# Optimization experiments

Hardware: AMD Instinct MI355X
Metric: run time of the kernel (lower is better)

Reference implementation:

```python
import jax, jax.numpy as jnp
import numpy as np

# dims
B, N, T, F, D = 16, 64, 168, 8, 248   # batch, stations, seq, features, gcn_dim
E = D + F                              # transformer dmodel = 256
H = 8                                  # attention heads
FF = 4 * E                             # expansion_factor * dmodel


def _layer_norm(x, g, b, eps=1e-5):
    m = jnp.mean(x, axis=-1, keepdims=True)
    v = jnp.var(x, axis=-1, keepdims=True)
    return (x - m) * jax.lax.rsqrt(v + eps) * g + b


def setup_inputs() -> dict:
    key = jax.random.key(0)
    ks = jax.random.split(key, 20)
    s = 0.02
    return {
        'x': jax.random.normal(ks[0], (B, N, T, F), jnp.float32),
        'locs': jax.random.uniform(ks[1], (B, N, 2), jnp.float32),
        'pos_em': jax.random.normal(ks[2], (B, T, E), jnp.float32),
        'periodic_em': jax.random.normal(ks[3], (B, T, E), jnp.float32),
        'gcn_w': jax.random.normal(ks[4], (F, D), jnp.float32) * s,
        'gcn_b': jnp.zeros((D,), jnp.float32),
        'fc1_w': jax.random.normal(ks[5], (D, D), jnp.float32) * s,
        'fc1_b': jnp.zeros((D,), jnp.float32),
        'wq': jax.random.normal(ks[6], (E, E), jnp.float32) * s,
        'bq': jnp.zeros((E,), jnp.float32),
        'wk': jax.random.normal(ks[7], (E, E), jnp.float32) * s,
        'bk': jnp.zeros((E,), jnp.float32),
        'wv': jax.random.normal(ks[8], (E, E), jnp.float32) * s,
        'bv': jnp.zeros((E,), jnp.float32),
        'wo': jax.random.normal(ks[9], (E, E), jnp.float32) * s,
        'bo': jnp.zeros((E,), jnp.float32),
        'ln1_g': jnp.ones((E,), jnp.float32),
        'ln1_b': jnp.zeros((E,), jnp.float32),
        'ln2_g': jnp.ones((E,), jnp.float32),
        'ln2_b': jnp.zeros((E,), jnp.float32),
        'ff1_w': jax.random.normal(ks[10], (E, FF), jnp.float32) * s,
        'ff1_b': jnp.zeros((FF,), jnp.float32),
        'ff2_w': jax.random.normal(ks[11], (FF, E), jnp.float32) * s,
        'ff2_b': jnp.zeros((E,), jnp.float32),
    }


def reference(x, locs, pos_em, periodic_em, gcn_w, gcn_b, fc1_w, fc1_b,
              wq, bq, wk, bk, wv, bv, wo, bo,
              ln1_g, ln1_b, ln2_g, ln2_b, ff1_w, ff1_b, ff2_w, ff2_b):
    b, n, t, f = x.shape
    # --- inverse-distance-weighted dense adjacency (fully connected graph) ---
    diff = locs[:, :, None, :] - locs[:, None, :, :]            # [B,N,N,2]
    dist = jnp.sqrt(jnp.sum(diff * diff, -1) + 1e-12)           # [B,N,N]
    w = jnp.where(jnp.eye(n, dtype=bool), 0.0, 1.0 / dist)      # no self edges
    w = w / jnp.sum(w, -1, keepdims=True)                       # norm=True
    # --- GCNConv (self loops + symmetric normalization), batched over B and T ---
    a = w + jnp.eye(n, dtype=x.dtype)
    dinv = jax.lax.rsqrt(jnp.sum(a, -1))
    a = a * dinv[:, :, None] * dinv[:, None, :]                 # [B,N,N]
    h = jnp.einsum('bntf,fd->bntd', x, gcn_w)                   # xW
    g = jax.nn.relu(jnp.einsum('bmn,bntd->bmtd', a, h) + gcn_b) # aggregate + relu
    g = jnp.einsum('bntd,de->bnte', g, fc1_w) + fc1_b           # fc1
    # --- concat features, flatten stations into batch, add positional embedding ---
    tok = jnp.concatenate([x, g], -1).reshape(b * n, t, -1)     # [B*N,T,E]
    tok = tok + jnp.repeat(pos_em, n, axis=0)                   # dropout=identity (eval)
    per = jnp.repeat(periodic_em, n, axis=0)
    # --- transformer encoder layer (periodic embedding conditions Q/K) ---
    e = tok.shape[-1]
    dh = e // H
    qk_in = tok + per
    q = (qk_in @ wq + bq).reshape(b * n, t, H, dh)
    k = (qk_in @ wk + bk).reshape(b * n, t, H, dh)
    v = (tok @ wv + bv).reshape(b * n, t, H, dh)
    s = jnp.einsum('bthd,bshd->bhts', q, k) * (1.0 / float(np.sqrt(dh)))
    p = jax.nn.softmax(s, axis=-1)
    o = jnp.einsum('bhts,bshd->bthd', p, v).reshape(b * n, t, e)
    o = o @ wo + bo
    h1 = _layer_norm(tok + o, ln1_g, ln1_b)
    ff = jax.nn.relu(h1 @ ff1_w + ff1_b) @ ff2_w + ff2_b
    out = _layer_norm(h1 + ff, ln2_g, ln2_b)
    return out.reshape(b, n, t, e)
```

## Files before the change

### kernel.cpp

```cpp
#include <hip/hip_runtime.h>
#include <hip/hip_bf16.h>

constexpr int B_  = 16;
constexpr int N_  = 64;
constexpr int T_  = 168;
constexpr int F_  = 8;
constexpr int E_  = 256;
constexpr int H_  = 8;
constexpr int DH_ = 32;
constexpr int NT_ = N_ * T_;
constexpr int LDQ_ = 768;

typedef __bf16 bf16x8 __attribute__((ext_vector_type(8)));
typedef float  f32x4  __attribute__((ext_vector_type(4)));
typedef float  f32x4u __attribute__((ext_vector_type(4), aligned(4)));

__device__ __forceinline__ unsigned short f2b(float f) {
  union { float f; unsigned int u; } v; v.f = f;
  unsigned int r = (v.u + 0x7FFFu + ((v.u >> 16) & 1u)) >> 16;
  return (unsigned short)r;
}
__device__ __forceinline__ float b2f(unsigned short h) {
  union { unsigned int u; float f; } v; v.u = ((unsigned int)h) << 16;
  return v.f;
}
__device__ __forceinline__ unsigned int cvtpk(float lo, float hi) {
  unsigned int r;
  asm("v_cvt_pk_bf16_f32 %0, %1, %2" : "=v"(r) : "v"(lo), "v"(hi));
  return r;
}
__device__ __forceinline__ void gload16(const void* g, void* l) {
  __builtin_amdgcn_global_load_lds(
      (const __attribute__((address_space(1))) unsigned int*)g,
      (__attribute__((address_space(3))) unsigned int*)l, 16, 0, 0);
}

__global__ void adj_kernel(const float* __restrict__ locs, float* __restrict__ a) {
  int b = blockIdx.x;
  int m = threadIdx.x;
  __shared__ float lx[64], ly[64];
  lx[m] = locs[(b * 64 + m) * 2 + 0];
  ly[m] = locs[(b * 64 + m) * 2 + 1];
  __syncthreads();
  float x = lx[m], y = ly[m];
  float sum = 0.f;
  for (int n = 0; n < 64; ++n) {
    float dx = x - lx[n], dy = y - ly[n];
    float d = sqrtf(dx * dx + dy * dy + 1e-12f);
    sum += (n == m) ? 0.f : 1.f / d;
  }
  float inv = 0.5f / sum;
  for (int n = 0; n < 64; ++n) {
    float dx = x - lx[n], dy = y - ly[n];
    float d = sqrtf(dx * dx + dy * dy + 1e-12f);
    float w = (n == m) ? 0.5f : inv / d;
    a[(b * 64 + m) * 64 + n] = w;
  }
}

__global__ void convw_kernel(const float* __restrict__ in, unsigned short* __restrict__ outT,
                             int K, int N, int Kp, int Np) {
  int idx = blockIdx.x * 256 + threadIdx.x;
  if (idx >= Np * Kp) return;
  int n = idx / Kp, k = idx % Kp;
  float v = (k < K && n < N) ? in[(long)k * N + n] : 0.f;
  outT[idx] = f2b(v);
}

__global__ __launch_bounds__(256) void gcn_kernel(
    const float* __restrict__ x, const float* __restrict__ adj,
    const float* __restrict__ gcn_w, const float* __restrict__ gcn_b,
    const float* __restrict__ pos_em, const float* __restrict__ per_em,
    unsigned short* __restrict__ G, unsigned short* __restrict__ tokb,
    unsigned short* __restrict__ qkb, int b0) {
  int bl = blockIdx.x / T_;
  int t = blockIdx.x % T_;
  int b = b0 + bl;
  int tid = threadIdx.x;
  __shared__ float sX[512];
  __shared__ float sXA[512];
  const float* adjb = adj + b * 4096;
  for (int i = tid; i < 512; i += 256) {
    int n = i >> 3, f = i & 7;
    sX[i] = x[((long)(b * 64 + n) * T_ + t) * F_ + f];
  }
  __syncthreads();
  for (int i = tid; i < 512; i += 256) {
    int m = i >> 3, f = i & 7;
    float s = 0.f;
    for (int n = 0; n < 64; ++n) s += adjb[(m << 6) + n] * sX[(n << 3) + f];
    sXA[i] = s;
  }
  {
    long pbase = ((long)bl * T_ + t) * E_;
    for (int i = tid; i < 512; i += 256) {
      int m = i >> 3, f = i & 7;
      long lrow = (long)(bl * 64 + m) * T_ + t;
      float base = sX[i] + pos_em[pbase + f];
      tokb[lrow * E_ + f] = f2b(base);
      qkb[lrow * E_ + f]  = f2b(base + per_em[pbase + f]);
    }
  }
  __syncthreads();
  for (int i = tid; i < 64 * 256; i += 256) {
    int m = i >> 8, d = i & 255;
    float v = 0.f;
    if (d < 248) {
      float s = gcn_b[d];
      const float* xam = &sXA[m << 3];
#pragma unroll
      for (int f = 0; f < 8; ++f) s += xam[f] * gcn_w[f * 248 + d];
      v = fmaxf(s, 0.f);
    }
    long lrow = (long)(bl * 64 + m) * T_ + t;
    G[lrow * 256 + d] = f2b(v);
  }
}

template <int KCHUNKS>
__global__ __launch_bounds__(256) void block_gemm(
    const unsigned short* __restrict__ A, int lda,
    const unsigned short* __restrict__ Bt, int K, int Nact,
    const float* __restrict__ bias,
    float* Cf, unsigned short* Cb1, unsigned short* Cb2,
    const float* __restrict__ emb1, const float* __restrict__ emb2,
    const unsigned short* __restrict__ resb, const float* resf,
    int c0, int ldc, int relu) {
  __shared__ unsigned short As[64 * 256];
  const int tid = threadIdx.x;
  const int lane = tid & 63, w = tid >> 6;
  const int l15 = lane & 15, lg = lane >> 4;
  const int m0 = blockIdx.x * 64;
  const int n0w = blockIdx.y * 256 + w * 64;

  f32x4 acc[4][4];
#pragma unroll
  for (int i = 0; i < 4; ++i)
#pragma unroll
    for (int j = 0; j < 4; ++j) acc[i][j] = (f32x4){0.f, 0.f, 0.f, 0.f};

  for (int kc = 0; kc < KCHUNKS; ++kc) {
    if (kc) __syncthreads();
#pragma unroll
    for (int j = 0; j < 8; ++j) {
      int idx = j * 256 + tid;
      int row = idx >> 5, g = idx & 31;
      int swg = (g & 24) | ((g & 7) ^ (row & 7));
      gload16(A + (long)(m0 + row) * lda + kc * 256 + swg * 8,
              &As[(j * 256 + w * 64) * 8]);
    }
    asm volatile("s_waitcnt vmcnt(0)" ::: "memory");
    __syncthreads();

#pragma unroll
    for (int ks = 0; ks < 8; ++ks) {
      bf16x8 Wf[4], Xf[4];
#pragma unroll
      for (int nf = 0; nf < 4; ++nf)
        Wf[nf] = *reinterpret_cast<const bf16x8*>(
            Bt + (long)(n0w + nf * 16 + l15) * K + kc * 256 + ks * 32 + (lg << 3));
#pragma unroll
      for (int mf = 0; mf < 4; ++mf) {
        int row = (mf << 4) + l15;
        int ksg = (ks << 2) + lg;
        int sw = (ksg & 24) | ((ksg & 7) ^ (row & 7));
        Xf[mf] = *reinterpret_cast<const bf16x8*>(&As[((row << 5) + sw) * 8]);
      }
#pragma unroll
      for (int mf = 0; mf < 4; ++mf)
#pragma unroll
        for (int nf = 0; nf < 4; ++nf)
          acc[mf][nf] = __builtin_amdgcn_mfma_f32_16x16x32_bf16(Wf[nf], Xf[mf], acc[mf][nf], 0, 0, 0);
    }
  }

  const int cb = lg << 2;
#pragma unroll
  for (int mf = 0; mf < 4; ++mf) {
    int rr = m0 + (mf << 4) + l15;
    int ar = (rr / NT_) * T_ + (rr % T_);
    long rbase  = (long)rr * ldc + c0;
    long rbase2 = (long)rr * 256 + c0;
    long abase  = (long)ar * 256 + c0;
#pragma unroll
    for (int nf = 0; nf < 4; ++nf) {
      int gcol = n0w + (nf << 4) + cb;
      if (gcol < Nact) {
        float v0 = acc[mf][nf][0], v1 = acc[mf][nf][1];
        float v2 = acc[mf][nf][2], v3 = acc[mf][nf][3];
        if (bias) {
          f32x4u b4 = *reinterpret_cast<const f32x4u*>(bias + gcol);
          v0 += b4[0]; v1 += b4[1]; v2 += b4[2]; v3 += b4[3];
        }
        if (relu) {
          v0 = fmaxf(v0, 0.f); v1 = fmaxf(v1, 0.f);
          v2 = fmaxf(v2, 0.f); v3 = fmaxf(v3, 0.f);
        }
        if (resb) {
          ushort4 rv = *reinterpret_cast<const ushort4*>(resb + rbase2 + gcol);
          v0 += b2f(rv.x); v1 += b2f(rv.y); v2 += b2f(rv.z); v3 += b2f(rv.w);
        }
        if (resf) {
          f32x4u r4 = *reinterpret_cast<const f32x4u*>(resf + rbase + gcol);
          v0 += r4[0]; v1 += r4[1]; v2 += r4[2]; v3 += r4[3];
        }
        if (emb1) {
          f32x4u e4 = *reinterpret_cast<const f32x4u*>(emb1 + abase + gcol);
          v0 += e4[0]; v1 += e4[1]; v2 += e4[2]; v3 += e4[3];
        }
        if (Cf) {
          f32x4u o; o[0] = v0; o[1] = v1; o[2] = v2; o[3] = v3;
          *reinterpret_cast<f32x4u*>(Cf + rbase + gcol) = o;
        }
        if (Cb1) {
          uint2 p = {cvtpk(v0, v1), cvtpk(v2, v3)};
          *reinterpret_cast<uint2*>(Cb1 + rbase + gcol) = p;
        }
        if (Cb2) {
          f32x4u e4 = *reinterpret_cast<const f32x4u*>(emb2 + abase + gcol);
          uint2 p = {cvtpk(v0 + e4[0], v1 + e4[1]), cvtpk(v2 + e4[2], v3 + e4[3])};
          *reinterpret_cast<uint2*>(Cb2 + rbase + gcol) = p;
        }
      }
    }
  }
}

__global__ __launch_bounds__(256) void ff_fused_kernel(
    const unsigned short* __restrict__ h1,
    const unsigned short* __restrict__ W1,
    const unsigned short* __restrict__ W2,
    const float* __restrict__ b1, const float* __restrict__ b2,
    unsigned short* __restrict__ outb) {
  __shared__ unsigned short h1s[64 * 256];
  __shared__ unsigned short fis[64 * 256];
  const int tid = threadIdx.x;
  const int lane = tid & 63, w = tid >> 6;
  const int l15 = lane & 15, lg = lane >> 4;
  const int m0 = blockIdx.x * 64;

#pragma unroll
  for (int j = 0; j < 8; ++j) {
    int idx = j * 256 + tid;
    int row = idx >> 5, g = idx & 31;
    int swg = (g & 24) | ((g & 7) ^ (row & 7));
    gload16(h1 + (long)(m0 + row) * 256 + swg * 8, &h1s[(j * 256 + w * 64) * 8]);
  }
  asm volatile("s_waitcnt vmcnt(0)" ::: "memory");
  __syncthreads();

  f32x4 acc2[4][4];
#pragma unroll
  for (int i = 0; i < 4; ++i)
#pragma unroll
    for (int j = 0; j < 4; ++j) acc2[i][j] = (f32x4){0.f, 0.f, 0.f, 0.f};

  const int cb = lg << 2;
  for (int nc = 0; nc < 4; ++nc) {
    f32x4 acc1[4][4];
#pragma unroll
    for (int i = 0; i < 4; ++i)
#pragma unroll
      for (int j = 0; j < 4; ++j) acc1[i][j] = (f32x4){0.f, 0.f, 0.f, 0.f};
#pragma unroll
    for (int ks = 0; ks < 8; ++ks) {
      bf16x8 Wf[4], Xf[4];
#pragma unroll
      for (int nf = 0; nf < 4; ++nf)
        Wf[nf] = *reinterpret_cast<const bf16x8*>(
            W1 + (long)(nc * 256 + w * 64 + nf * 16 + l15) * 256 + ks * 32 + (lg << 3));
#pragma unroll
      for (int mf = 0; mf < 4; ++mf) {
        int row = (mf << 4) + l15;
        int ksg = (ks << 2) + lg;
        int sw = (ksg & 24) | ((ksg & 7) ^ (row & 7));
        Xf[mf] = *reinterpret_cast<const bf16x8*>(&h1s[((row << 5) + sw) * 8]);
      }
#pragma unroll
      for (int mf = 0; mf < 4; ++mf)
#pragma unroll
        for (int nf = 0; nf < 4; ++nf)
          acc1[mf][nf] = __builtin_amdgcn_mfma_f32_16x16x32_bf16(Wf[nf], Xf[mf], acc1[mf][nf], 0, 0, 0);
    }
    if (nc) __syncthreads();
#pragma unroll
    for (int mf = 0; mf < 4; ++mf) {
      int row = (mf << 4) + l15;
#pragma unroll
      for (int nf = 0; nf < 4; ++nf) {
        int col = w * 64 + (nf << 4) + cb;
        f32x4u b4 = *reinterpret_cast<const f32x4u*>(b1 + nc * 256 + col);
        float v0 = fmaxf(acc1[mf][nf][0] + b4[0], 0.f);
        float v1 = fmaxf(acc1[mf][nf][1] + b4[1], 0.f);
        float v2 = fmaxf(acc1[mf][nf][2] + b4[2], 0.f);
        float v3 = fmaxf(acc1[mf][nf][3] + b4[3], 0.f);
        int g = col >> 3;
        int swg = (g & 24) | ((g & 7) ^ (row & 7));
        uint2 p = {cvtpk(v0, v1), cvtpk(v2, v3)};
        *reinterpret_cast<uint2*>(&fis[((row << 5) + swg) * 8 + (col & 7)]) = p;
      }
    }
    __syncthreads();
#pragma unroll
    for (int ks = 0; ks < 8; ++ks) {
      bf16x8 Wf[4], Xf[4];
#pragma unroll
      for (int nf = 0; nf < 4; ++nf)
        Wf[nf] = *reinterpret_cast<const bf16x8*>(
            W2 + (long)(w * 64 + nf * 16 + l15) * 1024 + nc * 256 + ks * 32 + (lg << 3));
#pragma unroll
      for (int mf = 0; mf < 4; ++mf) {
        int row = (mf << 4) + l15;
        int ksg = (ks << 2) + lg;
        int sw = (ksg & 24) | ((ksg & 7) ^ (row & 7));
        Xf[mf] = *reinterpret_cast<const bf16x8*>(&fis[((row << 5) + sw) * 8]);
      }
#pragma unroll
      for (int mf = 0; mf < 4; ++mf)
#pragma unroll
        for (int nf = 0; nf < 4; ++nf)
          acc2[mf][nf] = __builtin_amdgcn_mfma_f32_16x16x32_bf16(Wf[nf], Xf[mf], acc2[mf][nf], 0, 0, 0);
    }
  }

#pragma unroll
  for (int mf = 0; mf < 4; ++mf) {
    int row = (mf << 4) + l15;
    long rbase = (long)(m0 + row) * 256;
#pragma unroll
    for (int nf = 0; nf < 4; ++nf) {
      int gcol = w * 64 + (nf << 4) + cb;
      f32x4u b4 = *reinterpret_cast<const f32x4u*>(b2 + gcol);
      int g = gcol >> 3;
      int swg = (g & 24) | ((g & 7) ^ (row & 7));
      ushort4 rv = *reinterpret_cast<const ushort4*>(&h1s[((row << 5) + swg) * 8 + (gcol & 7)]);
      float v0 = acc2[mf][nf][0] + b4[0] + b2f(rv.x);
      float v1 = acc2[mf][nf][1] + b4[1] + b2f(rv.y);
      float v2 = acc2[mf][nf][2] + b4[2] + b2f(rv.z);
      float v3 = acc2[mf][nf][3] + b4[3] + b2f(rv.w);
      uint2 p = {cvtpk(v0, v1), cvtpk(v2, v3)};
      *reinterpret_cast<uint2*>(outb + rbase + gcol) = p;
    }
  }
}

__global__ __launch_bounds__(256) void attn_mfma_kernel(unsigned short* QKV) {
  int blk = blockIdx.x;
  int bn = blk >> 3, h = blk & 7;
  int tid = threadIdx.x;
  int lane = tid & 63, w = tid >> 6;

  __shared__ unsigned short Kfr[11 * 512];
  __shared__ unsigned short VT[32][200];
  __shared__ unsigned short Pb[4][16][200];

  const long qbase = (long)bn * T_ * LDQ_ + h * DH_;
  const unsigned short* Kg = QKV + qbase + 256;
  const unsigned short* V  = QKV + qbase + 512;
  const unsigned short* Q  = QKV + qbase;
  unsigned short* O = QKV + qbase;
  int l15 = lane & 15, lg = lane >> 4;

  for (int kt = w; kt < 11; kt += 4) {
    gload16(Kg + (long)(kt * 16 + l15) * LDQ_ + (lg << 3), &Kfr[kt * 512]);
  }
  for (int i = tid; i < T_ * 4; i += 256) {
    int t = i >> 2, seg = (i & 3) << 3;
    uint4 vv = *reinterpret_cast<const uint4*>(V + (long)t * LDQ_ + seg);
    const unsigned short* vs = (const unsigned short*)&vv;
#pragma unroll
    for (int j = 0; j < 8; ++j) VT[seg + j][t] = vs[j];
  }
  for (int i = tid; i < 32 * 32; i += 256) VT[i >> 5][168 + (i & 31)] = 0;
  {
    unsigned short* pflat = &Pb[0][0][0];
    for (int i = tid; i < 64 * 24; i += 256)
      pflat[(i / 24) * 200 + 176 + (i % 24)] = 0;
  }
  __syncthreads();

  const float scale = 0.17677669529663687f;
  unsigned short* Pw = &Pb[w][0][0];

  for (int it = 0; it < 3; ++it) {
    int qt = w + it * 4;
    if (qt > 10) break;
    bf16x8 af = *reinterpret_cast<const bf16x8*>(
        Q + (long)(qt * 16 + l15) * LDQ_ + (lg << 3));
    f32x4 s[11];
#pragma unroll
    for (int kt = 0; kt < 11; ++kt) {
      bf16x8 bf = *reinterpret_cast<const bf16x8*>(&Kfr[kt * 512 + lane * 8]);
      s[kt] = __builtin_amdgcn_mfma_f32_16x16x32_bf16(
          af, bf, (f32x4){0.f, 0.f, 0.f, 0.f}, 0, 0, 0);
    }
    bool ok10 = (l15 < 8);
    float inv_l[4];
#pragma unroll
    for (int r = 0; r < 4; ++r) {
      float mx = -1e30f;
#pragma unroll
      for (int kt = 0; kt < 10; ++kt) mx = fmaxf(mx, s[kt][r] * scale);
      if (ok10) mx = fmaxf(mx, s[10][r] * scale);
#pragma unroll
      for (int off = 1; off < 16; off <<= 1) mx = fmaxf(mx, __shfl_xor(mx, off, 64));
      float pv[11];
      float ls = 0.f;
#pragma unroll
      for (int kt = 0; kt < 11; ++kt) {
        bool valid = (kt < 10) || ok10;
        float p = valid ? __expf(s[kt][r] * scale - mx) : 0.f;
        pv[kt] = p;
        ls += p;
      }
#pragma unroll
      for (int off = 1; off < 16; off <<= 1) ls += __shfl_xor(ls, off, 64);
      inv_l[r] = 1.f / ls;
      int prow = (lg << 2) + r;
#pragma unroll
      for (int kt = 0; kt < 11; ++kt)
        Pw[prow * 200 + kt * 16 + l15] = f2b(pv[kt]);
    }
    asm volatile("s_waitcnt lgkmcnt(0)" ::: "memory");
    __builtin_amdgcn_sched_barrier(0);
    f32x4 o0 = (f32x4){0.f, 0.f, 0.f, 0.f};
    f32x4 o1 = (f32x4){0.f, 0.f, 0.f, 0.f};
#pragma unroll
    for (int ks = 0; ks < 6; ++ks) {
      bf16x8 pf = *reinterpret_cast<const bf16x8*>(&Pw[l15 * 200 + ks * 32 + (lg << 3)]);
      bf16x8 v0 = *reinterpret_cast<const bf16x8*>(&VT[l15][ks * 32 + (lg << 3)]);
      bf16x8 v1 = *reinterpret_cast<const bf16x8*>(&VT[16 + l15][ks * 32 + (lg << 3)]);
      o0 = __builtin_amdgcn_mfma_f32_16x16x32_bf16(pf, v0, o0, 0, 0, 0);
      o1 = __builtin_amdgcn_mfma_f32_16x16x32_bf16(pf, v1, o1, 0, 0, 0);
    }
    int rg = lg << 2;
#pragma unroll
    for (int r = 0; r < 4; ++r) {
      int q = qt * 16 + rg + r;
      if (q < T_) {
        long ob = (long)q * LDQ_;
        O[ob + l15]      = f2b(o0[r] * inv_l[r]);
        O[ob + 16 + l15] = f2b(o1[r] * inv_l[r]);
      }
    }
  }
}

__global__ __launch_bounds__(256) void ln_bf_kernel(
    const unsigned short* __restrict__ X, int ldx,
    const float* __restrict__ g, const float* __restrict__ bt,
    unsigned short* __restrict__ bout, float* __restrict__ fout) {
  long row = (long)blockIdx.x * 4 + (threadIdx.x >> 6);
  int lane = threadIdx.x & 63;
  ushort4 xv = *reinterpret_cast<const ushort4*>(X + row * ldx + (lane << 2));
  float v0 = b2f(xv.x), v1 = b2f(xv.y), v2 = b2f(xv.z), v3 = b2f(xv.w);
  float s = v0 + v1 + v2 + v3;
  float s2 = v0 * v0 + v1 * v1 + v2 * v2 + v3 * v3;
#pragma unroll
  for (int off = 32; off > 0; off >>= 1) {
    s += __shfl_xor(s, off, 64);
    s2 += __shfl_xor(s2, off, 64);
  }
  float mean = s * 0.00390625f;
  float var = s2 * 0.00390625f - mean * mean;
  float rs = rsqrtf(var + 1e-5f);
  float4 gv = *reinterpret_cast<const float4*>(g + (lane << 2));
  float4 bv = *reinterpret_cast<const float4*>(bt + (lane << 2));
  float o0 = (v0 - mean) * rs * gv.x + bv.x;
  float o1 = (v1 - mean) * rs * gv.y + bv.y;
  float o2 = (v2 - mean) * rs * gv.z + bv.z;
  float o3 = (v3 - mean) * rs * gv.w + bv.w;
  if (bout) {
    uint2 ov = {cvtpk(o0, o1), cvtpk(o2, o3)};
    *reinterpret_cast<uint2*>(bout + row * 256 + (lane << 2)) = ov;
  }
  if (fout) {
    float4 fo = {o0, o1, o2, o3};
    *reinterpret_cast<float4*>(fout + row * 256 + (lane << 2)) = fo;
  }
}

extern "C" void kernel_launch(void* const* d_in, const int* in_sizes, int n_in,
                              void* d_out, int out_size, void* d_ws, size_t ws_size,
                              hipStream_t stream) {
  const float* x      = (const float*)d_in[0];
  const float* locs   = (const float*)d_in[1];
  const float* pos_em = (const float*)d_in[2];
  const float* per_em = (const float*)d_in[3];
  const float* gcn_w  = (const float*)d_in[4];
  const float* gcn_b  = (const float*)d_in[5];
  const float* fc1_w  = (const float*)d_in[6];
  const float* fc1_b  = (const float*)d_in[7];
  const float* wq = (const float*)d_in[8];
  const float* bq = (const float*)d_in[9];
  const float* wk = (const float*)d_in[10];
  const float* bk = (const float*)d_in[11];
  const float* wv = (const float*)d_in[12];
  const float* bv = (const float*)d_in[13];
  const float* wo = (const float*)d_in[14];
  const float* bo = (const float*)d_in[15];
  const float* ln1_g = (const float*)d_in[16];
  const float* ln1_b = (const float*)d_in[17];
  const float* ln2_g = (const float*)d_in[18];
  const float* ln2_b = (const float*)d_in[19];
  const float* ff1_w = (const float*)d_in[20];
  const float* ff1_b = (const float*)d_in[21];
  const float* ff2_w = (const float*)d_in[22];
  const float* ff2_b = (const float*)d_in[23];
  float* out = (float*)d_out;

  const size_t ADJ_BYTES = 1u << 20;
  const size_t WB_BYTES  = 2u << 20;
  int CB = 16;
  while (CB > 1) {
    if (ADJ_BYTES + WB_BYTES + (size_t)CB * NT_ * 2560 <= ws_size) break;
    CB >>= 1;
  }
  char* ws = (char*)d_ws;
  float* adj = (float*)ws;
  unsigned short* wslab = (unsigned short*)(ws + ADJ_BYTES);
  unsigned short* fc1T  = wslab;
  unsigned short* wqkT  = wslab + 65536;
  unsigned short* wkT   = wslab + 2 * 65536;
  unsigned short* wvT   = wslab + 3 * 65536;
  unsigned short* woT   = wslab + 4 * 65536;
  unsigned short* ff1T  = wslab + 5 * 65536;
  unsigned short* ff2T  = wslab + 5 * 65536 + 262144;
  float* bqk = (float*)(ws + ADJ_BYTES + 1900544);

  unsigned short* tokb = (unsigned short*)(ws + ADJ_BYTES + WB_BYTES);
  unsigned short* qkb  = tokb + (size_t)CB * NT_ * 256;
  unsigned short* qkv  = qkb + (size_t)CB * NT_ * 256;
  unsigned short* h1b  = tokb;
  unsigned short* aob  = qkv + 256;

  adj_kernel<<<B_, 64, 0, stream>>>(locs, adj);
  convw_kernel<<<256, 256, 0, stream>>>(fc1_w, fc1T, 248, 248, 256, 256);
  convw_kernel<<<256, 256, 0, stream>>>(wq, wqkT, 256, 256, 256, 256);
  convw_kernel<<<256, 256, 0, stream>>>(wk, wkT, 256, 256, 256, 256);
  convw_kernel<<<256, 256, 0, stream>>>(wv, wvT, 256, 256, 256, 256);
  convw_kernel<<<256, 256, 0, stream>>>(wo, woT, 256, 256, 256, 256);
  convw_kernel<<<1024, 256, 0, stream>>>(ff1_w, ff1T, 256, 1024, 256, 1024);
  convw_kernel<<<1024, 256, 0, stream>>>(ff2_w, ff2T, 1024, 256, 1024, 256);
  hipMemcpyAsync(bqk, bq, 256 * sizeof(float), hipMemcpyDeviceToDevice, stream);
  hipMemcpyAsync(bqk + 256, bk, 256 * sizeof(float), hipMemcpyDeviceToDevice, stream);

  for (int b0 = 0; b0 < B_; b0 += CB) {
    const int rows = CB * NT_;
    const int GX = rows / 64;
    const float* pos_c = pos_em + (long)b0 * T_ * E_;
    const float* per_c = per_em + (long)b0 * T_ * E_;
    float* out_c = out + (long)b0 * NT_ * E_;
    unsigned short* G = qkv;

    gcn_kernel<<<CB * T_, 256, 0, stream>>>(x, adj, gcn_w, gcn_b, pos_c, per_c,
                                            G, tokb, qkb, b0);
    block_gemm<1><<<dim3(GX, 1), 256, 0, stream>>>(
        G, 256, fc1T, 256, 248, fc1_b, nullptr, tokb, qkb, pos_c, per_c,
        nullptr, nullptr, 8, 256, 0);
    block_gemm<1><<<dim3(GX, 2), 256, 0, stream>>>(
        qkb, 256, wqkT, 256, 512, bqk, nullptr, qkv, nullptr, nullptr, nullptr,
        nullptr, nullptr, 0, LDQ_, 0);
    block_gemm<1><<<dim3(GX, 1), 256, 0, stream>>>(
        tokb, 256, wvT, 256, 256, bv, nullptr, qkv, nullptr, nullptr, nullptr,
        nullptr, nullptr, 512, LDQ_, 0);
    attn_mfma_kernel<<<CB * N_ * H_, 256, 0, stream>>>(qkv);
    block_gemm<1><<<dim3(GX, 1), 256, 0, stream>>>(
        qkv, LDQ_, woT, 256, 256, bo, nullptr, aob, nullptr, nullptr, nullptr,
        tokb, nullptr, 0, LDQ_, 0);
    ln_bf_kernel<<<rows / 4, 256, 0, stream>>>(aob, LDQ_, ln1_g, ln1_b, h1b, nullptr);
    ff_fused_kernel<<<GX, 256, 0, stream>>>(h1b, ff1T, ff2T, ff1_b, ff2_b, h1b);
    ln_bf_kernel<<<rows / 4, 256, 0, stream>>>(h1b, 256, ln2_g, ln2_b, nullptr, out_c);
  }
}
```

Baseline: 1.246 ms.

## Fuse LayerNorms into the Wo GEMM and feed-forward kernel epilogues

```diff
diff --git a/kernel.cpp b/kernel.cpp
--- a/kernel.cpp
+++ b/kernel.cpp
@@ -226,21 +226,127 @@
   }
 }
 
+__global__ __launch_bounds__(256) void wo_ln_kernel(
+    const unsigned short* __restrict__ A, int lda,
+    const unsigned short* __restrict__ Wt,
+    const float* __restrict__ bias,
+    const unsigned short* __restrict__ resb,
+    const float* __restrict__ lng, const float* __restrict__ lnb,
+    unsigned short* __restrict__ outb) {
+  __shared__ unsigned short As[64 * 256];
+  __shared__ float red[4][4][16][2];
+  const int tid = threadIdx.x;
+  const int lane = tid & 63, w = tid >> 6;
+  const int l15 = lane & 15, lg = lane >> 4;
+  const int m0 = blockIdx.x * 64;
+  const int n0w = w * 64;
+
+  f32x4 acc[4][4];
+#pragma unroll
+  for (int i = 0; i < 4; ++i)
+#pragma unroll
+    for (int j = 0; j < 4; ++j) acc[i][j] = (f32x4){0.f, 0.f, 0.f, 0.f};
+
+#pragma unroll
+  for (int j = 0; j < 8; ++j) {
+    int idx = j * 256 + tid;
+    int row = idx >> 5, g = idx & 31;
+    int swg = (g & 24) | ((g & 7) ^ (row & 7));
+    gload16(A + (long)(m0 + row) * lda + swg * 8, &As[(j * 256 + w * 64) * 8]);
+  }
+  asm volatile("s_waitcnt vmcnt(0)" ::: "memory");
+  __syncthreads();
+
+#pragma unroll
+  for (int ks = 0; ks < 8; ++ks) {
+    bf16x8 Wf[4], Xf[4];
+#pragma unroll
+    for (int nf = 0; nf < 4; ++nf)
+      Wf[nf] = *reinterpret_cast<const bf16x8*>(
+          Wt + (long)(n0w + nf * 16 + l15) * 256 + ks * 32 + (lg << 3));
+#pragma unroll
+    for (int mf = 0; mf < 4; ++mf) {
+      int row = (mf << 4) + l15;
+      int ksg = (ks << 2) + lg;
+      int sw = (ksg & 24) | ((ksg & 7) ^ (row & 7));
+      Xf[mf] = *reinterpret_cast<const bf16x8*>(&As[((row << 5) + sw) * 8]);
+    }
+#pragma unroll
+    for (int mf = 0; mf < 4; ++mf)
+#pragma unroll
+      for (int nf = 0; nf < 4; ++nf)
+        acc[mf][nf] = __builtin_amdgcn_mfma_f32_16x16x32_bf16(Wf[nf], Xf[mf], acc[mf][nf], 0, 0, 0);
+  }
+
+  const int cb = lg << 2;
+  float s[4], s2[4];
+#pragma unroll
+  for (int mf = 0; mf < 4; ++mf) {
+    int rr = m0 + (mf << 4) + l15;
+    long rbase2 = (long)rr * 256;
+    s[mf] = 0.f; s2[mf] = 0.f;
+#pragma unroll
+    for (int nf = 0; nf < 4; ++nf) {
+      int gcol = n0w + (nf << 4) + cb;
+      f32x4u b4 = *reinterpret_cast<const f32x4u*>(bias + gcol);
+      ushort4 rv = *reinterpret_cast<const ushort4*>(resb + rbase2 + gcol);
+      float v0 = acc[mf][nf][0] + b4[0] + b2f(rv.x);
+      float v1 = acc[mf][nf][1] + b4[1] + b2f(rv.y);
+      float v2 = acc[mf][nf][2] + b4[2] + b2f(rv.z);
+      float v3 = acc[mf][nf][3] + b4[3] + b2f(rv.w);
+      acc[mf][nf][0] = v0; acc[mf][nf][1] = v1;
+      acc[mf][nf][2] = v2; acc[mf][nf][3] = v3;
+      s[mf] += v0 + v1 + v2 + v3;
+      s2[mf] += v0 * v0 + v1 * v1 + v2 * v2 + v3 * v3;
+    }
+    s[mf] += __shfl_xor(s[mf], 16, 64);
+    s[mf] += __shfl_xor(s[mf], 32, 64);
+    s2[mf] += __shfl_xor(s2[mf], 16, 64);
+    s2[mf] += __shfl_xor(s2[mf], 32, 64);
+    if (lg == 0) { red[w][mf][l15][0] = s[mf]; red[w][mf][l15][1] = s2[mf]; }
+  }
+  __syncthreads();
+#pragma unroll
+  for (int mf = 0; mf < 4; ++mf) {
+    float S  = red[0][mf][l15][0] + red[1][mf][l15][0] + red[2][mf][l15][0] + red[3][mf][l15][0];
+    float S2 = red[0][mf][l15][1] + red[1][mf][l15][1] + red[2][mf][l15][1] + red[3][mf][l15][1];
+    float mean = S * 0.00390625f;
+    float var = S2 * 0.00390625f - mean * mean;
+    float rs = rsqrtf(var + 1e-5f);
+    int rr = m0 + (mf << 4) + l15;
+    long rbase = (long)rr * 256;
+#pragma unroll
+    for (int nf = 0; nf < 4; ++nf) {
+      int gcol = n0w + (nf << 4) + cb;
+      f32x4u g4 = *reinterpret_cast<const f32x4u*>(lng + gcol);
+      f32x4u t4 = *reinterpret_cast<const f32x4u*>(lnb + gcol);
+      float o0 = (acc[mf][nf][0] - mean) * rs * g4[0] + t4[0];
+      float o1 = (acc[mf][nf][1] - mean) * rs * g4[1] + t4[1];
+      float o2 = (acc[mf][nf][2] - mean) * rs * g4[2] + t4[2];
+      float o3 = (acc[mf][nf][3] - mean) * rs * g4[3] + t4[3];
+      uint2 p = {cvtpk(o0, o1), cvtpk(o2, o3)};
+      *reinterpret_cast<uint2*>(outb + rbase + gcol) = p;
+    }
+  }
+}
+
 __global__ __launch_bounds__(256) void ff_fused_kernel(
     const unsigned short* __restrict__ h1,
     const unsigned short* __restrict__ W1,
     const unsigned short* __restrict__ W2,
     const float* __restrict__ b1, const float* __restrict__ b2,
-    unsigned short* __restrict__ outb) {
-  __shared__ unsigned short h1s[64 * 256];
-  __shared__ unsigned short fis[64 * 256];
+    const float* __restrict__ lng, const float* __restrict__ lnb,
+    float* __restrict__ out) {
+  __shared__ unsigned short h1s[32 * 256];
+  __shared__ unsigned short fis[32 * 256];
+  __shared__ float red[4][2][16][2];
   const int tid = threadIdx.x;
   const int lane = tid & 63, w = tid >> 6;
   const int l15 = lane & 15, lg = lane >> 4;
-  const int m0 = blockIdx.x * 64;
-
-#pragma unroll
-  for (int j = 0; j < 8; ++j) {
+  const int m0 = blockIdx.x * 32;
+
+#pragma unroll
+  for (int j = 0; j < 4; ++j) {
     int idx = j * 256 + tid;
     int row = idx >> 5, g = idx & 31;
     int swg = (g & 24) | ((g & 7) ^ (row & 7));
@@ -249,42 +355,42 @@
   asm volatile("s_waitcnt vmcnt(0)" ::: "memory");
   __syncthreads();
 
-  f32x4 acc2[4][4];
-#pragma unroll
-  for (int i = 0; i < 4; ++i)
+  f32x4 acc2[2][4];
+#pragma unroll
+  for (int i = 0; i < 2; ++i)
 #pragma unroll
     for (int j = 0; j < 4; ++j) acc2[i][j] = (f32x4){0.f, 0.f, 0.f, 0.f};
 
   const int cb = lg << 2;
   for (int nc = 0; nc < 4; ++nc) {
-    f32x4 acc1[4][4];
-#pragma unroll
-    for (int i = 0; i < 4; ++i)
+    f32x4 acc1[2][4];
+#pragma unroll
+    for (int i = 0; i < 2; ++i)
 #pragma unroll
       for (int j = 0; j < 4; ++j) acc1[i][j] = (f32x4){0.f, 0.f, 0.f, 0.f};
 #pragma unroll
     for (int ks = 0; ks < 8; ++ks) {
-      bf16x8 Wf[4], Xf[4];
+      bf16x8 Wf[4], Xf[2];
 #pragma unroll
       for (int nf = 0; nf < 4; ++nf)
         Wf[nf] = *reinterpret_cast<const bf16x8*>(
             W1 + (long)(nc * 256 + w * 64 + nf * 16 + l15) * 256 + ks * 32 + (lg << 3));
 #pragma unroll
-      for (int mf = 0; mf < 4; ++mf) {
+      for (int mf = 0; mf < 2; ++mf) {
         int row = (mf << 4) + l15;
         int ksg = (ks << 2) + lg;
         int sw = (ksg & 24) | ((ksg & 7) ^ (row & 7));
         Xf[mf] = *reinterpret_cast<const bf16x8*>(&h1s[((row << 5) + sw) * 8]);
       }
 #pragma unroll
-      for (int mf = 0; mf < 4; ++mf)
+      for (int mf = 0; mf < 2; ++mf)
 #pragma unroll
         for (int nf = 0; nf < 4; ++nf)
           acc1[mf][nf] = __builtin_amdgcn_mfma_f32_16x16x32_bf16(Wf[nf], Xf[mf], acc1[mf][nf], 0, 0, 0);
     }
     if (nc) __syncthreads();
 #pragma unroll
-    for (int mf = 0; mf < 4; ++mf) {
+    for (int mf = 0; mf < 2; ++mf) {
       int row = (mf << 4) + l15;
 #pragma unroll
       for (int nf = 0; nf < 4; ++nf) {
@@ -303,30 +409,31 @@
     __syncthreads();
 #pragma unroll
     for (int ks = 0; ks < 8; ++ks) {
-      bf16x8 Wf[4], Xf[4];
+      bf16x8 Wf[4], Xf[2];
 #pragma unroll
       for (int nf = 0; nf < 4; ++nf)
         Wf[nf] = *reinterpret_cast<const bf16x8*>(
             W2 + (long)(w * 64 + nf * 16 + l15) * 1024 + nc * 256 + ks * 32 + (lg << 3));
 #pragma unroll
-      for (int mf = 0; mf < 4; ++mf) {
+      for (int mf = 0; mf < 2; ++mf) {
         int row = (mf << 4) + l15;
         int ksg = (ks << 2) + lg;
         int sw = (ksg & 24) | ((ksg & 7) ^ (row & 7));
         Xf[mf] = *reinterpret_cast<const bf16x8*>(&fis[((row << 5) + sw) * 8]);
       }
 #pragma unroll
-      for (int mf = 0; mf < 4; ++mf)
+      for (int mf = 0; mf < 2; ++mf)
 #pragma unroll
         for (int nf = 0; nf < 4; ++nf)
           acc2[mf][nf] = __builtin_amdgcn_mfma_f32_16x16x32_bf16(Wf[nf], Xf[mf], acc2[mf][nf], 0, 0, 0);
     }
   }
 
-#pragma unroll
-  for (int mf = 0; mf < 4; ++mf) {
+  float s[2], s2[2];
+#pragma unroll
+  for (int mf = 0; mf < 2; ++mf) {
     int row = (mf << 4) + l15;
-    long rbase = (long)(m0 + row) * 256;
+    s[mf] = 0.f; s2[mf] = 0.f;
 #pragma unroll
     for (int nf = 0; nf < 4; ++nf) {
       int gcol = w * 64 + (nf << 4) + cb;
@@ -338,8 +445,38 @@
       float v1 = acc2[mf][nf][1] + b4[1] + b2f(rv.y);
       float v2 = acc2[mf][nf][2] + b4[2] + b2f(rv.z);
       float v3 = acc2[mf][nf][3] + b4[3] + b2f(rv.w);
-      uint2 p = {cvtpk(v0, v1), cvtpk(v2, v3)};
-      *reinterpret_cast<uint2*>(outb + rbase + gcol) = p;
+      acc2[mf][nf][0] = v0; acc2[mf][nf][1] = v1;
+      acc2[mf][nf][2] = v2; acc2[mf][nf][3] = v3;
+      s[mf] += v0 + v1 + v2 + v3;
+      s2[mf] += v0 * v0 + v1 * v1 + v2 * v2 + v3 * v3;
+    }
+    s[mf] += __shfl_xor(s[mf], 16, 64);
+    s[mf] += __shfl_xor(s[mf], 32, 64);
+    s2[mf] += __shfl_xor(s2[mf], 16, 64);
+    s2[mf] += __shfl_xor(s2[mf], 32, 64);
+    if (lg == 0) { red[w][mf][l15][0] = s[mf]; red[w][mf][l15][1] = s2[mf]; }
+  }
+  __syncthreads();
+#pragma unroll
+  for (int mf = 0; mf < 2; ++mf) {
+    float S  = red[0][mf][l15][0] + red[1][mf][l15][0] + red[2][mf][l15][0] + red[3][mf][l15][0];
+    float S2 = red[0][mf][l15][1] + red[1][mf][l15][1] + red[2][mf][l15][1] + red[3][mf][l15][1];
+    float mean = S * 0.00390625f;
+    float var = S2 * 0.00390625f - mean * mean;
+    float rs = rsqrtf(var + 1e-5f);
+    int rr = m0 + (mf << 4) + l15;
+    long rbase = (long)rr * 256;
+#pragma unroll
+    for (int nf = 0; nf < 4; ++nf) {
+      int gcol = w * 64 + (nf << 4) + cb;
+      f32x4u g4 = *reinterpret_cast<const f32x4u*>(lng + gcol);
+      f32x4u t4 = *reinterpret_cast<const f32x4u*>(lnb + gcol);
+      f32x4u o;
+      o[0] = (acc2[mf][nf][0] - mean) * rs * g4[0] + t4[0];
+      o[1] = (acc2[mf][nf][1] - mean) * rs * g4[1] + t4[1];
+      o[2] = (acc2[mf][nf][2] - mean) * rs * g4[2] + t4[2];
+      o[3] = (acc2[mf][nf][3] - mean) * rs * g4[3] + t4[3];
+      *reinterpret_cast<f32x4u*>(out + rbase + gcol) = o;
     }
   }
 }
@@ -443,40 +580,6 @@
         O[ob + 16 + l15] = f2b(o1[r] * inv_l[r]);
       }
     }
-  }
-}
-
-__global__ __launch_bounds__(256) void ln_bf_kernel(
-    const unsigned short* __restrict__ X, int ldx,
-    const float* __restrict__ g, const float* __restrict__ bt,
-    unsigned short* __restrict__ bout, float* __restrict__ fout) {
-  long row = (long)blockIdx.x * 4 + (threadIdx.x >> 6);
-  int lane = threadIdx.x & 63;
-  ushort4 xv = *reinterpret_cast<const ushort4*>(X + row * ldx + (lane << 2));
-  float v0 = b2f(xv.x), v1 = b2f(xv.y), v2 = b2f(xv.z), v3 = b2f(xv.w);
-  float s = v0 + v1 + v2 + v3;
-  float s2 = v0 * v0 + v1 * v1 + v2 * v2 + v3 * v3;
-#pragma unroll
-  for (int off = 32; off > 0; off >>= 1) {
-    s += __shfl_xor(s, off, 64);
-    s2 += __shfl_xor(s2, off, 64);
-  }
-  float mean = s * 0.00390625f;
-  float var = s2 * 0.00390625f - mean * mean;
-  float rs = rsqrtf(var + 1e-5f);
-  float4 gv = *reinterpret_cast<const float4*>(g + (lane << 2));
-  float4 bv = *reinterpret_cast<const float4*>(bt + (lane << 2));
-  float o0 = (v0 - mean) * rs * gv.x + bv.x;
-  float o1 = (v1 - mean) * rs * gv.y + bv.y;
-  float o2 = (v2 - mean) * rs * gv.z + bv.z;
-  float o3 = (v3 - mean) * rs * gv.w + bv.w;
-  if (bout) {
-    uint2 ov = {cvtpk(o0, o1), cvtpk(o2, o3)};
-    *reinterpret_cast<uint2*>(bout + row * 256 + (lane << 2)) = ov;
-  }
-  if (fout) {
-    float4 fo = {o0, o1, o2, o3};
-    *reinterpret_cast<float4*>(fout + row * 256 + (lane << 2)) = fo;
   }
 }
 
@@ -532,7 +635,6 @@
   unsigned short* qkb  = tokb + (size_t)CB * NT_ * 256;
   unsigned short* qkv  = qkb + (size_t)CB * NT_ * 256;
   unsigned short* h1b  = tokb;
-  unsigned short* aob  = qkv + 256;
 
   adj_kernel<<<B_, 64, 0, stream>>>(locs, adj);
   convw_kernel<<<256, 256, 0, stream>>>(fc1_w, fc1T, 248, 248, 256, 256);
@@ -565,11 +667,9 @@
         tokb, 256, wvT, 256, 256, bv, nullptr, qkv, nullptr, nullptr, nullptr,
         nullptr, nullptr, 512, LDQ_, 0);
     attn_mfma_kernel<<<CB * N_ * H_, 256, 0, stream>>>(qkv);
-    block_gemm<1><<<dim3(GX, 1), 256, 0, stream>>>(
-        qkv, LDQ_, woT, 256, 256, bo, nullptr, aob, nullptr, nullptr, nullptr,
-        tokb, nullptr, 0, LDQ_, 0);
-    ln_bf_kernel<<<rows / 4, 256, 0, stream>>>(aob, LDQ_, ln1_g, ln1_b, h1b, nullptr);
-    ff_fused_kernel<<<GX, 256, 0, stream>>>(h1b, ff1T, ff2T, ff1_b, ff2_b, h1b);
-    ln_bf_kernel<<<rows / 4, 256, 0, stream>>>(h1b, 256, ln2_g, ln2_b, nullptr, out_c);
-  }
-}
+    wo_ln_kernel<<<GX, 256, 0, stream>>>(qkv, LDQ_, woT, bo, tokb,
+                                         ln1_g, ln1_b, h1b);
+    ff_fused_kernel<<<rows / 32, 256, 0, stream>>>(h1b, ff1T, ff2T, ff1_b, ff2_b,
+                                                   ln2_g, ln2_b, out_c);
+  }
+}
```

New measurement: 1.428 ms. +14.6%, slower.
